# Kernel tuning notes

Hardware: AMD Instinct MI355X
Metric: run time of the kernel (lower is better)

Reference implementation:

```python
import jax, jax.numpy as jnp
import numpy as np

SEQ, B, OBS, H = 128, 256, 64, 1024

def setup_inputs() -> dict:
    key = jax.random.key(0)
    ks = jax.random.split(key, 16)
    s = 0.03  # keep weights small so tanh/sigmoid stay in a sane range
    n = lambda k, shape, sc=s: jax.random.normal(k, shape, jnp.float32) * sc
    return {
        "x": jax.random.normal(ks[0], (SEQ * B, OBS), jnp.float32),
        "done": jax.random.randint(ks[1], (SEQ * B,), 0, 2).astype(jnp.int32),
        "h0": n(ks[2], (2, B, H), 0.1),
        "c0": n(ks[3], (2, B, H), 0.1),
        "W_ih0": n(ks[4], (4 * H, OBS)),
        "W_hh0": n(ks[5], (4 * H, H)),
        "b_ih0": jnp.zeros((4 * H,), jnp.float32),
        "b_hh0": jnp.zeros((4 * H,), jnp.float32),
        "W_ih1": n(ks[6], (4 * H, H)),
        "W_hh1": n(ks[7], (4 * H, H)),
        "b_ih1": jnp.zeros((4 * H,), jnp.float32),
        "b_hh1": jnp.zeros((4 * H,), jnp.float32),
        "ln_g": jnp.ones((H,), jnp.float32),
        "ln_b": jnp.zeros((H,), jnp.float32),
        "W1": n(ks[8], (512, H)),
        "b1": jnp.zeros((512,), jnp.float32),
        "W2": n(ks[9], (128, 512)),
        "b2": jnp.zeros((128,), jnp.float32),
        "W3": n(ks[10], (64, 128)),
        "b3": jnp.zeros((64,), jnp.float32),
        "Wv": n(ks[11], (1, 64)),
        "bv": jnp.zeros((1,), jnp.float32),
    }

def _lstm_cell(xin, h, c, Wih, Whh, bih, bhh):
    # PyTorch gate order: input, forget, cell(g), output
    g = xin @ Wih.T + bih + h @ Whh.T + bhh
    i, f, gg, o = jnp.split(g, 4, axis=-1)
    c2 = jax.nn.sigmoid(f) * c + jax.nn.sigmoid(i) * jnp.tanh(gg)
    h2 = jax.nn.sigmoid(o) * jnp.tanh(c2)
    return h2, c2

def reference(x, done, h0, c0, W_ih0, W_hh0, b_ih0, b_hh0, W_ih1, W_hh1,
              b_ih1, b_hh1, ln_g, ln_b, W1, b1, W2, b2, W3, b3, Wv, bv):
    batch = h0.shape[1]
    obs = x.shape[-1]
    xs = x.reshape(-1, batch, obs)                      # (S, B, obs)
    ds = done.reshape(-1, batch).astype(x.dtype)        # (S, B)

    def step(carry, td):
        h, c = carry                                    # each (2, B, H)
        xt, dt = td
        m = (1.0 - dt)[:, None]                         # reset mask (B, 1)
        h0_, c0_ = _lstm_cell(xt, h[0] * m, c[0] * m, W_ih0, W_hh0, b_ih0, b_hh0)
        h1_, c1_ = _lstm_cell(h0_, h[1] * m, c[1] * m, W_ih1, W_hh1, b_ih1, b_hh1)
        return (jnp.stack([h0_, h1_]), jnp.stack([c0_, c1_])), h1_

    (hN, cN), hs = jax.lax.scan(step, (h0, c0), (xs, ds))
    hidden = hs.reshape(-1, hs.shape[-1])               # (S*B, H)

    # LayerNorm (eps = 1e-5, torch default)
    mu = hidden.mean(-1, keepdims=True)
    var = jnp.mean(jnp.square(hidden - mu), -1, keepdims=True)
    hn = (hidden - mu) * jax.lax.rsqrt(var + 1e-5) * ln_g + ln_b

    a = jax.nn.elu(hn @ W1.T + b1)
    a = jax.nn.elu(a @ W2.T + b2)
    a = jax.nn.elu(a @ W3.T + b3)
    value = a @ Wv.T + bv                               # (S*B, 1)
    return value, hN, cN
```

## Files before the change

### kernel.cpp

```cpp
#include <hip/hip_runtime.h>
#include <cstdint>
#include <cstddef>

typedef unsigned short u16;
typedef __attribute__((ext_vector_type(8))) short short8;
typedef __attribute__((ext_vector_type(4))) float f32x4;

#define SEQ 128
#define BATCH 256
#define HID 1024
#define LSZ 262144
#define RING 8

#define MFMA(a,b,c) __builtin_amdgcn_mfma_f32_16x16x32_bf16((a),(b),(c),0,0,0)

__device__ __forceinline__ u16 f2b(float f) {
  union { float f; unsigned u; } v; v.f = f;
  unsigned r = (v.u + 0x7FFFu + ((v.u >> 16) & 1u)) >> 16;
  return (u16)r;
}
__device__ __forceinline__ float b2f(u16 h) {
  union { unsigned u; float f; } v; v.u = ((unsigned)h) << 16; return v.f;
}
__device__ __forceinline__ float sigm(float x){ return 1.f/(1.f + __expf(-x)); }
__device__ __forceinline__ float tanh_f(float x){
  x = fminf(15.f, fmaxf(-15.f, x));
  float e = __expf(2.f*x); return (e-1.f)/(e+1.f);
}
__device__ __forceinline__ float eluf(float x){ return x > 0.f ? x : expm1f(x); }

__device__ __forceinline__ void gload(const u16* p, short8& d) {
  asm volatile("global_load_dwordx4 %0, %1, off" : "=&v"(d) : "v"(p) : "memory");
}
__device__ __forceinline__ void gload_nt(const u16* p, short8& d) {
  asm volatile("global_load_dwordx4 %0, %1, off nt" : "=&v"(d) : "v"(p) : "memory");
}
__device__ __forceinline__ void gload_cg(const u16* p, short8& d) {
  asm volatile("global_load_dwordx4 %0, %1, off sc0 sc1" : "=&v"(d) : "v"(p) : "memory");
}
__device__ __forceinline__ void store_cg(u16* p, short8 v) {
  asm volatile("global_store_dwordx4 %0, %1, off sc0 sc1" :: "v"(p), "v"(v) : "memory");
}
__device__ __forceinline__ void wait_vm0() {
  asm volatile("s_waitcnt vmcnt(0)" ::: "memory");
}
__device__ __forceinline__ void flag_set(int* p, int val) {
  asm volatile("global_store_dword %0, %1, off sc0 sc1" :: "v"(p), "v"(val) : "memory");
}
__device__ __forceinline__ void waitgroup(const int* f, int tgt) {
  if (threadIdx.x < 32) {
    const int* p = f + threadIdx.x * 32;
    while (true) {
      int v;
      asm volatile("global_load_dword %0, %1, off sc0 sc1\n\ts_waitcnt vmcnt(0)"
                   : "=v"(v) : "v"(p) : "memory");
      if (v >= tgt) break;
      __builtin_amdgcn_s_sleep(1);
    }
  }
  __syncthreads();
}

#define TIES_VB(vB) "+v"(vB[0][0]),"+v"(vB[0][1]),"+v"(vB[0][2]),"+v"(vB[0][3]), \
                    "+v"(vB[1][0]),"+v"(vB[1][1]),"+v"(vB[1][2]),"+v"(vB[1][3]), \
                    "+v"(vB[2][0]),"+v"(vB[2][1]),"+v"(vB[2][2]),"+v"(vB[2][3]), \
                    "+v"(vB[3][0]),"+v"(vB[3][1]),"+v"(vB[3][2]),"+v"(vB[3][3])
#define TIES_SV "+v"(sv[0]),"+v"(sv[1]),"+v"(sv[2]),"+v"(sv[3]),"+v"(sv[4]),"+v"(sv[5]),"+v"(sv[6]),"+v"(sv[7])

static const size_t OFF_W0F  = 0;
static const size_t OFF_W1F  = 8912896;
static const size_t OFF_XF   = 25690112;
static const size_t OFF_FLG  = 30932992;
static const size_t OFF_H1U  = 33030144;
static const size_t OFF_BS0  = 100663296;
static const size_t OFF_BS1  = 100679680;
static const size_t OFF_MU   = 100697088;
static const size_t OFF_RSTD = 100828160;
static const size_t OFF_W1LN = 100959232;
static const size_t OFF_S1   = 102007808;
static const size_t OFF_B1P  = 102009856;
static const size_t OFF_W2B  = 102011904;
static const size_t OFF_W3B  = 102142976;
static const size_t OFF_A1   = 102159360;
static const size_t OFF_H0R  = 102159360;
static const size_t OFF_A2   = 0;
static const size_t OFF_A3   = 8912896;

__global__ void prep_wf(const float* __restrict__ wih, const float* __restrict__ whh,
                        u16* __restrict__ out, int nkb, int kx) {
  int b = blockIdx.x; int cg = b >> 3, ct = b & 7;
  int g = ct >> 1;
  int n = nkb << 9;
  for (int e = threadIdx.x; e < n; e += 256) {
    int kb = e >> 9, r = e & 511;
    int q = r >> 7, col16 = (r >> 3) & 15, j = r & 7;
    int hl = (ct & 1) * 16 + col16;
    int gr = g * HID + cg * 32 + hl;
    int k = kb * 32 + q * 8 + j;
    float w = (k < kx) ? wih[(size_t)gr * kx + k] : whh[(size_t)gr * HID + (k - kx)];
    out[((size_t)(cg * nkb + kb) * 8 + ct) * 512 + r] = f2b(w);
  }
}

__global__ void prep_w1ln(const float* __restrict__ w1, const float* __restrict__ lng,
                          const float* __restrict__ lnb, const float* __restrict__ b1,
                          u16* __restrict__ w1ln, float* __restrict__ S1, float* __restrict__ b1p) {
  int j = blockIdx.x;
  float s = 0.f, bb = 0.f;
  for (int k = threadIdx.x; k < HID; k += 256) {
    float w = w1[(size_t)j * HID + k];
    u16 q = f2b(w * lng[k]);
    w1ln[(size_t)j * HID + k] = q;
    s += b2f(q);
    bb += w * lnb[k];
  }
  __shared__ float r1[256], r2[256];
  r1[threadIdx.x] = s; r2[threadIdx.x] = bb;
  __syncthreads();
  for (int o = 128; o > 0; o >>= 1) {
    if (threadIdx.x < (unsigned)o) { r1[threadIdx.x] += r1[threadIdx.x+o]; r2[threadIdx.x] += r2[threadIdx.x+o]; }
    __syncthreads();
  }
  if (threadIdx.x == 0) { S1[j] = r1[0]; b1p[j] = b1[j] + r2[0]; }
}

__global__ void prep_misc(const float* bih0, const float* bhh0, const float* bih1, const float* bhh1,
                          const float* x, const float* h0in,
                          const float* w2, const float* w3,
                          float* bs0, float* bs1, u16* xf, u16* h0r, u16* h1u,
                          u16* w2b, u16* w3b, int* flg) {
  size_t i = (size_t)blockIdx.x * blockDim.x + threadIdx.x;
  if (i < 4096) { bs0[i] = bih0[i] + bhh0[i]; return; }
  i -= 4096;
  if (i < 4096) { bs1[i] = bih1[i] + bhh1[i]; return; }
  i -= 4096;
  if (i < 2097152) {
    int o = (int)i;
    int r = o & 511, tile = o >> 9;
    int q = r >> 7, rl = (r >> 3) & 15, j = r & 7;
    int kb = tile & 1, v = tile >> 1;
    int grt = v & 15, t = v >> 4;
    int row = grt * 16 + rl, k = kb * 32 + q * 8 + j;
    xf[o] = f2b(x[((size_t)t * BATCH + row) * 64 + k]);
    return;
  }
  i -= 2097152;
  if (i < 262144) {
    int o = (int)i;
    int r = o & 511, tile = o >> 9;
    int q = r >> 7, rl = (r >> 3) & 15, j = r & 7;
    int grt = tile >> 5, kb = tile & 31;
    int row = grt * 16 + rl, h = kb * 32 + q * 8 + j;
    h0r[o] = f2b(h0in[(size_t)row * HID + h]);
    return;
  }
  i -= 262144;
  if (i < 262144) {
    int o = (int)i;
    int r = o & 511, tile = o >> 9;
    int q = r >> 7, rl = (r >> 3) & 15, j = r & 7;
    int grt = tile >> 5, kb = tile & 31;
    int row = grt * 16 + rl, h = kb * 32 + q * 8 + j;
    h1u[o] = f2b(h0in[LSZ + (size_t)row * HID + h]);
    return;
  }
  i -= 262144;
  if (i < 65536) { w2b[i] = f2b(w2[i]); return; }
  i -= 65536;
  if (i < 8192) { w3b[i] = f2b(w3[i]); return; }
  i -= 8192;
  if (i < 256) { flg[i * 32] = 0; return; }
}

__global__ __launch_bounds__(256, 1) void lstm_persist(
    const u16* __restrict__ w0f, const u16* __restrict__ w1f, const u16* __restrict__ xf,
    u16* __restrict__ h0r, u16* __restrict__ h1u,
    const float* __restrict__ c0all,
    const float* __restrict__ bs0, const float* __restrict__ bs1,
    const int* __restrict__ done, int* __restrict__ flg,
    float* __restrict__ dout)
{
  const int bid = blockIdx.x;
  const int layer = bid >> 7;
  const int rg = (bid >> 5) & 3;
  const int cg = bid & 31;
  const int tid = threadIdx.x;
  const int lane = tid & 63, wv = tid >> 6;
  const int wgr = wv & 1, wgc = wv >> 1;
  const int quad = lane >> 4, c16 = lane & 15;
  const int NKB = layer ? 64 : 34;
  const int NC  = layer ? 8 : 5;
  const int NH  = layer ? 16 : 9;
  const u16* Wf = layer ? w1f : w0f;
  const float* bs = layer ? bs1 : bs0;
  const float* cb = c0all + (size_t)layer * LSZ;
  int* fl0 = flg;
  int* fl1 = flg + 128 * 32;
  int* myf = (layer ? fl1 : fl0) + (rg * 32 + cg) * 32;
  int* g0 = fl0 + rg * 32 * 32;
  int* g1 = fl1 + rg * 32 * 32;

  __shared__ __align__(16) u16 smem[32768];
  float* gl = (float*)smem;

  const int sgrt = rg * 4 + wv;
  const int woff = (lane >> 4) * 128 + (lane & 15) * 8;
  const int srow = rg * 64 + wv * 16 + (lane & 15);
  const short8 z8 = {0,0,0,0,0,0,0,0};

  float creg[8];
  {
    const float* cp0 = cb + (size_t)(rg * 64 + (tid >> 2)) * HID + cg * 32 + (tid & 3) * 8;
    #pragma unroll
    for (int j = 0; j < 8; ++j) creg[j] = cp0[j];
  }

  for (int t = 0; t < SEQ; ++t) {
    if (layer == 0) {
      if (t >= RING) waitgroup(g1, t - (RING - 1));
      if (t >= 1)    waitgroup(g0, t);
    } else {
      waitgroup(g0, t + 1);
    }

    int sdone = done[t * BATCH + srow];
    asm volatile("" : "+v"(sdone));

    f32x4 acc0[4], acc1[4];
    #pragma unroll
    for (int i = 0; i < 4; ++i) { acc0[i] = (f32x4){0,0,0,0}; acc1[i] = (f32x4){0,0,0,0}; }
    short8 sv[8];
    short8 vBa[4][4], vBb[4][4];

    auto issueA = [&](int c) {
      int kb0 = c * 8;
      #pragma unroll
      for (int kbl = 0; kbl < 8; ++kbl) {
        int kb = kb0 + kbl;
        if (kb > NKB - 1) kb = NKB - 1;
        if (layer == 0) {
          if (kb < 2) {
            gload_nt(xf + ((size_t)((t * 16 + sgrt) * 2 + kb)) * 512 + woff, sv[kbl]);
          } else {
            gload_cg(h0r + (size_t)(t & (RING-1)) * 262144 + (size_t)(sgrt * 32 + (kb - 2)) * 512 + woff, sv[kbl]);
          }
        } else {
          if (kb < 32) {
            gload_cg(h0r + (size_t)((t + 1) & (RING-1)) * 262144 + (size_t)(sgrt * 32 + kb) * 512 + woff, sv[kbl]);
          } else {
            gload(h1u + (size_t)t * 262144 + (size_t)(sgrt * 32 + (kb - 32)) * 512 + woff, sv[kbl]);
          }
        }
      }
    };
    auto commitA = [&](int c) {
      int kb0 = c * 8;
      int bo = (c & 1) << 14;
      u16* d = &smem[bo + wv * 512 + woff];
      #pragma unroll
      for (int kbl = 0; kbl < 8; ++kbl) {
        int kb = kb0 + kbl;
        int maskable = layer ? (kb >= 32) : (kb >= 2);
        short8 v = sv[kbl];
        if (maskable && sdone) v = z8;
        *(short8*)(d + kbl * 2048) = v;
      }
    };
    auto issueB = [&](int h, short8 (&vB)[4][4]) {
      int kk = h * 4;
      #pragma unroll
      for (int kbl = 0; kbl < 4; ++kbl) {
        int kbx = kk + kbl;
        if (kbx > NKB - 1) kbx = NKB - 1;
        #pragma unroll
        for (int ct = 0; ct < 4; ++ct)
          gload(Wf + ((size_t)(cg * NKB + kbx) * 8 + wgc * 4 + ct) * 512 + lane * 8, vB[kbl][ct]);
      }
    };
    auto comp4 = [&](int h, short8 (&vB)[4][4]) {
      int kbc4 = NKB - h * 4; if (kbc4 > 4) kbc4 = 4;
      int bo = ((h >> 1) & 1) << 14;
      int tb = (h & 1) * 4;
      #pragma unroll
      for (int kbl = 0; kbl < 4; ++kbl) if (kbl < kbc4) {
        short8 af0 = *(const short8*)&smem[bo + ((tb + kbl) * 4 + wgr * 2 + 0) * 512 + lane * 8];
        short8 af1 = *(const short8*)&smem[bo + ((tb + kbl) * 4 + wgr * 2 + 1) * 512 + lane * 8];
        #pragma unroll
        for (int ct = 0; ct < 4; ++ct) {
          acc0[ct] = MFMA(af0, vB[kbl][ct], acc0[ct]);
          acc1[ct] = MFMA(af1, vB[kbl][ct], acc1[ct]);
        }
      }
    };

    issueB(0, vBa);
    issueA(0);
    issueB(1, vBb);
    asm volatile("s_waitcnt vmcnt(16)" : TIES_SV, TIES_VB(vBa) :: "memory");
    __builtin_amdgcn_sched_barrier(0);
    commitA(0);
    __syncthreads();

    for (int c = 0; c < NC - 1; ++c) {
      if (layer && c == 3 && t >= 1) waitgroup(g1, t);
      issueA(c + 1);
      comp4(2 * c, vBa);
      issueB(2 * c + 2, vBa);
      asm volatile("s_waitcnt vmcnt(24)" : TIES_VB(vBb) :: "memory");
      __builtin_amdgcn_sched_barrier(0);
      comp4(2 * c + 1, vBb);
      issueB(2 * c + 3, vBb);
      asm volatile("s_waitcnt vmcnt(32)" : TIES_SV :: "memory");
      __builtin_amdgcn_sched_barrier(0);
      commitA(c + 1);
      asm volatile("s_waitcnt vmcnt(16)" : TIES_VB(vBa) :: "memory");
      __builtin_amdgcn_sched_barrier(0);
      __syncthreads();
    }
    {
      int c = NC - 1;
      comp4(2 * c, vBa);
      asm volatile("s_waitcnt vmcnt(0)" : TIES_VB(vBb) :: "memory");
      __builtin_amdgcn_sched_barrier(0);
      if (2 * c + 1 < NH) comp4(2 * c + 1, vBb);
      __syncthreads();
    }

    #pragma unroll
    for (int ct = 0; ct < 4; ++ct)
      #pragma unroll
      for (int rgi = 0; rgi < 4; ++rgi) {
        int row0 = wgr * 32 + quad * 4 + rgi;
        int col = wgc * 64 + ct * 16 + c16;
        gl[row0 * 128 + col] = acc0[ct][rgi];
        gl[(row0 + 16) * 128 + col] = acc1[ct][rgi];
      }
    __syncthreads();

    {
      int row = tid >> 2;
      int q = tid & 3;
      int h8 = q * 8;
      int rowg = rg * 64 + row;
      int H0 = cg * 32 + h8;
      const float* glp = gl + row * 128;
      float m = done[t * BATCH + rowg] ? 0.f : 1.f;
      short8 hv;
      float h2a[8];
      #pragma unroll
      for (int j = 0; j < 8; ++j) {
        float ivv = glp[h8 + j]      + bs[H0 + j];
        float fvv = glp[32 + h8 + j] + bs[HID + H0 + j];
        float gvv = glp[64 + h8 + j] + bs[2*HID + H0 + j];
        float ovv = glp[96 + h8 + j] + bs[3*HID + H0 + j];
        float c2 = sigm(fvv) * (creg[j] * m) + sigm(ivv) * tanh_f(gvv);
        float h2 = sigm(ovv) * tanh_f(c2);
        creg[j] = c2;
        h2a[j] = h2;
        ((u16*)&hv)[j] = f2b(h2);
      }
      size_t off = (size_t)((rg * 4 + (row >> 4)) * 32 + cg) * 512 + (size_t)(q * 16 + (row & 15)) * 8;
      if (layer == 0) store_cg(h0r + (size_t)((t + 1) & (RING-1)) * 262144 + off, hv);
      else            store_cg(h1u + (size_t)(t + 1) * 262144 + off, hv);
      if (t == SEQ - 1) {
        float* dh = dout + 32768 + (size_t)layer * LSZ + (size_t)rowg * HID + H0;
        float* dc = dout + 32768 + 2 * LSZ + (size_t)layer * LSZ + (size_t)rowg * HID + H0;
        #pragma unroll
        for (int j = 0; j < 8; ++j) { dh[j] = h2a[j]; dc[j] = creg[j]; }
      }
    }
    wait_vm0();
    __syncthreads();
    if (tid == 0) flag_set(myf, t + 1);
  }
}

__global__ void ln_stats(const u16* __restrict__ h1u, float* __restrict__ mu, float* __restrict__ rstd) {
  int R = blockIdx.x * 4 + (threadIdx.x >> 6);
  int l = threadIdx.x & 63;
  int t = R >> 8, brow = R & 255, grt = brow >> 4, rl = brow & 15;
  const u16* base = h1u + (size_t)(t + 1) * 262144 + (size_t)(grt * 32 + (l >> 1)) * 512;
  int q2 = (l & 1) * 2;
  short8 v0 = *(const short8*)(base + (q2 * 16 + rl) * 8);
  short8 v1 = *(const short8*)(base + ((q2 + 1) * 16 + rl) * 8);
  float s = 0.f, q = 0.f;
  #pragma unroll
  for (int e = 0; e < 8; ++e) {
    float a = b2f((u16)v0[e]); s += a; q += a*a;
    float b = b2f((u16)v1[e]); s += b; q += b*b;
  }
  for (int o = 32; o > 0; o >>= 1) { s += __shfl_xor(s, o); q += __shfl_xor(q, o); }
  if (l == 0) {
    float mm = s * (1.f/1024.f);
    float var = q * (1.f/1024.f) - mm*mm;
    mu[R] = mm; rstd[R] = rsqrtf(var + 1e-5f);
  }
}

__global__ __launch_bounds__(512, 4) void mlp_gemm(
    const u16* __restrict__ A, int lda, int amode,
    const u16* __restrict__ B, int K, int N,
    u16* __restrict__ out, int ldo, int mode, int swiz,
    const float* __restrict__ mu, const float* __restrict__ rstd,
    const float* __restrict__ S1v, const float* __restrict__ bias)
{
  int nt, mtb;
  if (swiz) { int p = blockIdx.x * gridDim.y + blockIdx.y; nt = p & 3; mtb = p >> 2; }
  else { nt = blockIdx.x; mtb = blockIdx.y; }
  const int tid = threadIdx.x, lane = tid & 63, wv = tid >> 6;
  const int quad = lane >> 4, c16 = lane & 15;
  __shared__ __align__(16) u16 Am[16384], Bm[16384];
  f32x4 acc[8];
  #pragma unroll
  for (int i = 0; i < 8; ++i) acc[i] = (f32x4){0.f,0.f,0.f,0.f};

  int arow[4], akl[4], bcol[4];
  #pragma unroll
  for (int i = 0; i < 4; ++i) {
    int s = tid + i * 512, sub = s >> 6, lp = s & 63;
    int ks = sub >> 3, u = sub & 7;
    arow[i] = mtb * 128 + u * 16 + (lp & 15);
    akl[i]  = ks * 32 + (lp >> 4) * 8;
    bcol[i] = nt * 128 + u * 16 + (lp & 15);
  }
  short8 vA[4], vB[4];
  const short8 z8 = {0,0,0,0,0,0,0,0};
  const int NCH = K >> 7;
  auto load_stage = [&](int ci) {
    int kc = ci << 7;
    #pragma unroll
    for (int i = 0; i < 4; ++i) {
      if (amode) {
        int R = arow[i], k = kc + akl[i];
        const u16* p = A + (size_t)((R >> 8) + 1) * 262144
                         + (size_t)(((R >> 4) & 15) * 32 + (k >> 5)) * 512
                         + (size_t)((((k >> 3) & 3) * 16 + (R & 15)) * 8);
        vA[i] = *(const short8*)p;
      } else {
        vA[i] = *(const short8*)(A + (size_t)arow[i] * lda + kc + akl[i]);
      }
      vB[i] = (bcol[i] < N) ? *(const short8*)(B + (size_t)bcol[i] * K + kc + akl[i]) : z8;
    }
  };
  load_stage(0);
  for (int ci = 0; ci < NCH; ++ci) {
    #pragma unroll
    for (int i = 0; i < 4; ++i) {
      *(short8*)&Am[(size_t)(tid + i*512) * 8] = vA[i];
      *(short8*)&Bm[(size_t)(tid + i*512) * 8] = vB[i];
    }
    __syncthreads();
    if (ci + 1 < NCH) load_stage(ci + 1);
    #pragma unroll
    for (int ks = 0; ks < 4; ++ks) {
      short8 bf = *(const short8*)&Bm[((ks*8 + wv)*64 + lane) * 8];
      #pragma unroll
      for (int rt = 0; rt < 8; ++rt) {
        short8 af = *(const short8*)&Am[((ks*8 + rt)*64 + lane) * 8];
        acc[rt] = MFMA(af, bf, acc[rt]);
      }
    }
    __syncthreads();
  }
  int col = nt * 128 + wv * 16 + c16;
  if (col < N) {
    #pragma unroll
    for (int rt = 0; rt < 8; ++rt) {
      #pragma unroll
      for (int rgi = 0; rgi < 4; ++rgi) {
        int row = mtb * 128 + rt * 16 + quad * 4 + rgi;
        float v = acc[rt][rgi];
        if (mode == 0) v = v * rstd[row] - mu[row] * rstd[row] * S1v[col] + bias[col];
        else           v = v + bias[col];
        v = eluf(v);
        out[(size_t)row * ldo + col] = f2b(v);
      }
    }
  }
}

__global__ void value_head(const u16* __restrict__ a3, const float* __restrict__ wv,
                           const float* __restrict__ bv, float* __restrict__ dout) {
  int row = blockIdx.x * 256 + threadIdx.x;
  const short8* p = (const short8*)(a3 + (size_t)row * 64);
  float s = bv[0];
  #pragma unroll
  for (int j = 0; j < 8; ++j) {
    short8 v = p[j];
    #pragma unroll
    for (int e = 0; e < 8; ++e) s += b2f((u16)v[e]) * wv[j*8+e];
  }
  dout[row] = s;
}

extern "C" void kernel_launch(void* const* d_in, const int* in_sizes, int n_in,
                              void* d_out, int out_size, void* d_ws, size_t ws_size,
                              hipStream_t stream) {
  (void)in_sizes; (void)n_in; (void)out_size; (void)ws_size;
  const float* x    = (const float*)d_in[0];
  const int*   done = (const int*)d_in[1];
  const float* h0in = (const float*)d_in[2];
  const float* c0in = (const float*)d_in[3];
  const float* wih0 = (const float*)d_in[4];
  const float* whh0 = (const float*)d_in[5];
  const float* bih0 = (const float*)d_in[6];
  const float* bhh0 = (const float*)d_in[7];
  const float* wih1 = (const float*)d_in[8];
  const float* whh1 = (const float*)d_in[9];
  const float* bih1 = (const float*)d_in[10];
  const float* bhh1 = (const float*)d_in[11];
  const float* lng  = (const float*)d_in[12];
  const float* lnb  = (const float*)d_in[13];
  const float* w1   = (const float*)d_in[14];
  const float* b1   = (const float*)d_in[15];
  const float* w2   = (const float*)d_in[16];
  const float* b2   = (const float*)d_in[17];
  const float* w3   = (const float*)d_in[18];
  const float* b3   = (const float*)d_in[19];
  const float* wvp  = (const float*)d_in[20];
  const float* bvp  = (const float*)d_in[21];
  float* dout = (float*)d_out;
  char* ws = (char*)d_ws;

  u16*   w0f  = (u16*)(ws + OFF_W0F);
  u16*   w1f  = (u16*)(ws + OFF_W1F);
  u16*   xf   = (u16*)(ws + OFF_XF);
  u16*   h0r  = (u16*)(ws + OFF_H0R);
  u16*   h1u  = (u16*)(ws + OFF_H1U);
  float* bs0  = (float*)(ws + OFF_BS0);
  float* bs1  = (float*)(ws + OFF_BS1);
  int*   flg  = (int*)(ws + OFF_FLG);
  float* mu   = (float*)(ws + OFF_MU);
  float* rstd = (float*)(ws + OFF_RSTD);
  u16*   w1ln = (u16*)(ws + OFF_W1LN);
  float* s1   = (float*)(ws + OFF_S1);
  float* b1p  = (float*)(ws + OFF_B1P);
  u16*   w2b  = (u16*)(ws + OFF_W2B);
  u16*   w3b  = (u16*)(ws + OFF_W3B);
  u16*   a1   = (u16*)(ws + OFF_A1);
  u16*   a2   = (u16*)(ws + OFF_A2);
  u16*   a3   = (u16*)(ws + OFF_A3);

  prep_wf<<<256, 256, 0, stream>>>(wih0, whh0, w0f, 34, 64);
  prep_wf<<<256, 256, 0, stream>>>(wih1, whh1, w1f, 64, 1024);
  prep_w1ln<<<512, 256, 0, stream>>>(w1, lng, lnb, b1, w1ln, s1, b1p);
  prep_misc<<<12609, 256, 0, stream>>>(bih0, bhh0, bih1, bhh1, x, h0in, w2, w3,
                                       bs0, bs1, xf, h0r, h1u, w2b, w3b, flg);

  lstm_persist<<<256, 256, 0, stream>>>(w0f, w1f, xf, h0r, h1u, c0in,
                                        bs0, bs1, done, flg, dout);

  ln_stats<<<8192, 256, 0, stream>>>(h1u, mu, rstd);
  mlp_gemm<<<dim3(8, 128), 512, 0, stream>>>(h1u, 0, 1, w1ln, 1024, 512, a1, 512, 0, 1, mu, rstd, s1, b1p);
  mlp_gemm<<<dim3(1, 256), 512, 0, stream>>>(a1, 512, 0, w2b, 512, 128, a2, 128, 1, 0, mu, rstd, s1, b2);
  mlp_gemm<<<dim3(1, 256), 512, 0, stream>>>(a2, 128, 0, w3b, 128, 64, a3, 64, 1, 0, mu, rstd, s1, b3);
  value_head<<<128, 256, 0, stream>>>(a3, wvp, bvp, dout);
}
```

Baseline: 2.950 ms.

## Double LDS stage size to 16 k-blocks and halve per-timestep barriers

Restructures the per-timestep K loop of the persistent LSTM kernel so each LDS stage holds 16 k-blocks instead of 8. Shared memory doubles to 128 KB, which halves the number of __syncthreads per timestep, and the A-operand loads are split into two halves interleaved with the weight loads and MFMA groups. The aim is to cut barrier overhead and improve overlap of global loads with compute. In exchange, LDS occupancy rises and the vmcnt wait accounting becomes more intricate: issueB past the last k-block is clamped, and the final stage issues redundant loads.

```diff
diff --git a/kernel.cpp b/kernel.cpp
--- a/kernel.cpp
+++ b/kernel.cpp
@@ -65,7 +65,6 @@
                     "+v"(vB[1][0]),"+v"(vB[1][1]),"+v"(vB[1][2]),"+v"(vB[1][3]), \
                     "+v"(vB[2][0]),"+v"(vB[2][1]),"+v"(vB[2][2]),"+v"(vB[2][3]), \
                     "+v"(vB[3][0]),"+v"(vB[3][1]),"+v"(vB[3][2]),"+v"(vB[3][3])
-#define TIES_SV "+v"(sv[0]),"+v"(sv[1]),"+v"(sv[2]),"+v"(sv[3]),"+v"(sv[4]),"+v"(sv[5]),"+v"(sv[6]),"+v"(sv[7])
 
 static const size_t OFF_W0F  = 0;
 static const size_t OFF_W1F  = 8912896;
@@ -189,8 +188,7 @@
   const int wgr = wv & 1, wgc = wv >> 1;
   const int quad = lane >> 4, c16 = lane & 15;
   const int NKB = layer ? 64 : 34;
-  const int NC  = layer ? 8 : 5;
-  const int NH  = layer ? 16 : 9;
+  const int NC2 = layer ? 4 : 3;
   const u16* Wf = layer ? w1f : w0f;
   const float* bs = layer ? bs1 : bs0;
   const float* cb = c0all + (size_t)layer * LSZ;
@@ -200,13 +198,13 @@
   int* g0 = fl0 + rg * 32 * 32;
   int* g1 = fl1 + rg * 32 * 32;
 
-  __shared__ __align__(16) u16 smem[32768];
+  __shared__ __align__(16) u16 smem[65536];
   float* gl = (float*)smem;
 
   const int sgrt = rg * 4 + wv;
   const int woff = (lane >> 4) * 128 + (lane & 15) * 8;
-  const int srow = rg * 64 + wv * 16 + (lane & 15);
   const short8 z8 = {0,0,0,0,0,0,0,0};
+  (void)z8;
 
   float creg[8];
   {
@@ -223,7 +221,7 @@
       waitgroup(g0, t + 1);
     }
 
-    int sdone = done[t * BATCH + srow];
+    int sdone = done[t * BATCH + (rg * 64 + wv * 16 + (lane & 15))];
     asm volatile("" : "+v"(sdone));
 
     f32x4 acc0[4], acc1[4];
@@ -232,8 +230,8 @@
     short8 sv[8];
     short8 vBa[4][4], vBb[4][4];
 
-    auto issueA = [&](int c) {
-      int kb0 = c * 8;
+    auto issueA = [&](int c, int p) {
+      int kb0 = c * 16 + p * 8;
       #pragma unroll
       for (int kbl = 0; kbl < 8; ++kbl) {
         int kb = kb0 + kbl;
@@ -253,16 +251,16 @@
         }
       }
     };
-    auto commitA = [&](int c) {
-      int kb0 = c * 8;
-      int bo = (c & 1) << 14;
-      u16* d = &smem[bo + wv * 512 + woff];
+    auto commitA = [&](int c, int p) {
+      int kb0 = c * 16 + p * 8;
+      int bo = (c & 1) << 15;
+      u16* d = &smem[bo + (p * 32 + wv) * 512 + woff];
       #pragma unroll
       for (int kbl = 0; kbl < 8; ++kbl) {
         int kb = kb0 + kbl;
         int maskable = layer ? (kb >= 32) : (kb >= 2);
         short8 v = sv[kbl];
-        if (maskable && sdone) v = z8;
+        if (maskable && sdone) v = (short8){0,0,0,0,0,0,0,0};
         *(short8*)(d + kbl * 2048) = v;
       }
     };
@@ -279,8 +277,8 @@
     };
     auto comp4 = [&](int h, short8 (&vB)[4][4]) {
       int kbc4 = NKB - h * 4; if (kbc4 > 4) kbc4 = 4;
-      int bo = ((h >> 1) & 1) << 14;
-      int tb = (h & 1) * 4;
+      int bo = ((h >> 2) & 1) << 15;
+      int tb = (h & 3) * 4;
       #pragma unroll
       for (int kbl = 0; kbl < 4; ++kbl) if (kbl < kbc4) {
         short8 af0 = *(const short8*)&smem[bo + ((tb + kbl) * 4 + wgr * 2 + 0) * 512 + lane * 8];
@@ -293,36 +291,41 @@
       }
     };
 
+    issueA(0, 0);
     issueB(0, vBa);
-    issueA(0);
+    asm volatile("s_waitcnt vmcnt(16)" ::: "memory");
+    __builtin_amdgcn_sched_barrier(0);
+    commitA(0, 0);
+    issueA(0, 1);
     issueB(1, vBb);
-    asm volatile("s_waitcnt vmcnt(16)" : TIES_SV, TIES_VB(vBa) :: "memory");
+    asm volatile("s_waitcnt vmcnt(16)" : TIES_VB(vBa) :: "memory");
     __builtin_amdgcn_sched_barrier(0);
-    commitA(0);
+    commitA(0, 1);
     __syncthreads();
 
-    for (int c = 0; c < NC - 1; ++c) {
-      if (layer && c == 3 && t >= 1) waitgroup(g1, t);
-      issueA(c + 1);
-      comp4(2 * c, vBa);
-      issueB(2 * c + 2, vBa);
+    for (int c = 0; c < NC2; ++c) {
+      if (layer && c == 1 && t >= 1) waitgroup(g1, t);
+      int pre = (c + 1 < NC2);
+      comp4(4 * c, vBa);
+      issueB(4 * c + 2, vBa);
+      issueA(c + 1, 0);
       asm volatile("s_waitcnt vmcnt(24)" : TIES_VB(vBb) :: "memory");
       __builtin_amdgcn_sched_barrier(0);
-      comp4(2 * c + 1, vBb);
-      issueB(2 * c + 3, vBb);
-      asm volatile("s_waitcnt vmcnt(32)" : TIES_SV :: "memory");
-      __builtin_amdgcn_sched_barrier(0);
-      commitA(c + 1);
+      comp4(4 * c + 1, vBb);
+      issueB(4 * c + 3, vBb);
       asm volatile("s_waitcnt vmcnt(16)" : TIES_VB(vBa) :: "memory");
       __builtin_amdgcn_sched_barrier(0);
-      __syncthreads();
-    }
-    {
-      int c = NC - 1;
-      comp4(2 * c, vBa);
-      asm volatile("s_waitcnt vmcnt(0)" : TIES_VB(vBb) :: "memory");
+      if (pre) commitA(c + 1, 0);
+      issueA(c + 1, 1);
+      comp4(4 * c + 2, vBa);
+      issueB(4 * c + 4, vBa);
+      asm volatile("s_waitcnt vmcnt(16)" : TIES_VB(vBb) :: "memory");
       __builtin_amdgcn_sched_barrier(0);
-      if (2 * c + 1 < NH) comp4(2 * c + 1, vBb);
+      if (pre) commitA(c + 1, 1);
+      comp4(4 * c + 3, vBb);
+      issueB(4 * c + 5, vBb);
+      asm volatile("s_waitcnt vmcnt(16)" : TIES_VB(vBa) :: "memory");
+      __builtin_amdgcn_sched_barrier(0);
       __syncthreads();
     }
 
```

After: 3.091 ms. +4.8%, slower.

## Stage LSTM weight tiles into LDS via global_load_lds and rebalance wave tiling

Applied to the files above, without the earlier changes.

Recurrent weight fragments are now loaded straight from global memory into a double-buffered LDS region with global_load_lds, instead of into registers held across iterations. The wave layout also changes: each wave now owns 2 column tiles across all 4 row tiles, reading A from LDS per row tile. The goal is to cut register pressure and simplify the prefetch pipeline. The cost is double the shared memory, extra LDS reads per MFMA, and a pipeline where B staging depends on vmcnt and lgkmcnt waits. Those waits, the loop now running NC iterations, and cross-wave LDS visibility all risk races or stalls.

```diff
diff --git a/kernel.cpp b/kernel.cpp
--- a/kernel.cpp
+++ b/kernel.cpp
@@ -29,14 +29,19 @@
 }
 __device__ __forceinline__ float eluf(float x){ return x > 0.f ? x : expm1f(x); }
 
+__device__ __forceinline__ void gload_nt(const u16* p, short8& d) {
+  asm volatile("global_load_dwordx4 %0, %1, off nt" : "=&v"(d) : "v"(p) : "memory");
+}
+__device__ __forceinline__ void gload_cg(const u16* p, short8& d) {
+  asm volatile("global_load_dwordx4 %0, %1, off sc0 sc1" : "=&v"(d) : "v"(p) : "memory");
+}
 __device__ __forceinline__ void gload(const u16* p, short8& d) {
   asm volatile("global_load_dwordx4 %0, %1, off" : "=&v"(d) : "v"(p) : "memory");
 }
-__device__ __forceinline__ void gload_nt(const u16* p, short8& d) {
-  asm volatile("global_load_dwordx4 %0, %1, off nt" : "=&v"(d) : "v"(p) : "memory");
-}
-__device__ __forceinline__ void gload_cg(const u16* p, short8& d) {
-  asm volatile("global_load_dwordx4 %0, %1, off sc0 sc1" : "=&v"(d) : "v"(p) : "memory");
+__device__ __forceinline__ void gll16(const u16* gsrc, u16* ldst) {
+  __builtin_amdgcn_global_load_lds(
+      (const __attribute__((address_space(1))) unsigned int*)(const void*)gsrc,
+      (__attribute__((address_space(3))) unsigned int*)(void*)ldst, 16, 0, 0);
 }
 __device__ __forceinline__ void store_cg(u16* p, short8 v) {
   asm volatile("global_store_dwordx4 %0, %1, off sc0 sc1" :: "v"(p), "v"(v) : "memory");
@@ -61,10 +66,6 @@
   __syncthreads();
 }
 
-#define TIES_VB(vB) "+v"(vB[0][0]),"+v"(vB[0][1]),"+v"(vB[0][2]),"+v"(vB[0][3]), \
-                    "+v"(vB[1][0]),"+v"(vB[1][1]),"+v"(vB[1][2]),"+v"(vB[1][3]), \
-                    "+v"(vB[2][0]),"+v"(vB[2][1]),"+v"(vB[2][2]),"+v"(vB[2][3]), \
-                    "+v"(vB[3][0]),"+v"(vB[3][1]),"+v"(vB[3][2]),"+v"(vB[3][3])
 #define TIES_SV "+v"(sv[0]),"+v"(sv[1]),"+v"(sv[2]),"+v"(sv[3]),"+v"(sv[4]),"+v"(sv[5]),"+v"(sv[6]),"+v"(sv[7])
 
 static const size_t OFF_W0F  = 0;
@@ -186,11 +187,9 @@
   const int cg = bid & 31;
   const int tid = threadIdx.x;
   const int lane = tid & 63, wv = tid >> 6;
-  const int wgr = wv & 1, wgc = wv >> 1;
   const int quad = lane >> 4, c16 = lane & 15;
   const int NKB = layer ? 64 : 34;
   const int NC  = layer ? 8 : 5;
-  const int NH  = layer ? 16 : 9;
   const u16* Wf = layer ? w1f : w0f;
   const float* bs = layer ? bs1 : bs0;
   const float* cb = c0all + (size_t)layer * LSZ;
@@ -200,13 +199,14 @@
   int* g0 = fl0 + rg * 32 * 32;
   int* g1 = fl1 + rg * 32 * 32;
 
-  __shared__ __align__(16) u16 smem[32768];
+  __shared__ __align__(16) u16 smem[65536];
   float* gl = (float*)smem;
+  u16* smemB = smem + 32768;
 
   const int sgrt = rg * 4 + wv;
   const int woff = (lane >> 4) * 128 + (lane & 15) * 8;
-  const int srow = rg * 64 + wv * 16 + (lane & 15);
   const short8 z8 = {0,0,0,0,0,0,0,0};
+  (void)z8;
 
   float creg[8];
   {
@@ -223,14 +223,13 @@
       waitgroup(g0, t + 1);
     }
 
-    int sdone = done[t * BATCH + srow];
+    int sdone = done[t * BATCH + (rg * 64 + wv * 16 + (lane & 15))];
     asm volatile("" : "+v"(sdone));
 
-    f32x4 acc0[4], acc1[4];
-    #pragma unroll
-    for (int i = 0; i < 4; ++i) { acc0[i] = (f32x4){0,0,0,0}; acc1[i] = (f32x4){0,0,0,0}; }
+    f32x4 acc[4][2];
+    #pragma unroll
+    for (int i = 0; i < 4; ++i) { acc[i][0] = (f32x4){0,0,0,0}; acc[i][1] = (f32x4){0,0,0,0}; }
     short8 sv[8];
-    short8 vBa[4][4], vBb[4][4];
 
     auto issueA = [&](int c) {
       int kb0 = c * 8;
@@ -262,79 +261,74 @@
         int kb = kb0 + kbl;
         int maskable = layer ? (kb >= 32) : (kb >= 2);
         short8 v = sv[kbl];
-        if (maskable && sdone) v = z8;
+        if (maskable && sdone) v = (short8){0,0,0,0,0,0,0,0};
         *(short8*)(d + kbl * 2048) = v;
       }
     };
-    auto issueB = [&](int h, short8 (&vB)[4][4]) {
+    auto stageB = [&](int h) {
+      int sb = ((h & 1) << 14) + (wv << 12);
       int kk = h * 4;
       #pragma unroll
       for (int kbl = 0; kbl < 4; ++kbl) {
         int kbx = kk + kbl;
         if (kbx > NKB - 1) kbx = NKB - 1;
         #pragma unroll
-        for (int ct = 0; ct < 4; ++ct)
-          gload(Wf + ((size_t)(cg * NKB + kbx) * 8 + wgc * 4 + ct) * 512 + lane * 8, vB[kbl][ct]);
+        for (int ctl = 0; ctl < 2; ++ctl)
+          gll16(Wf + ((size_t)(cg * NKB + kbx) * 8 + wv * 2 + ctl) * 512 + lane * 8,
+                &smemB[sb + (kbl * 2 + ctl) * 512]);
       }
     };
-    auto comp4 = [&](int h, short8 (&vB)[4][4]) {
+    auto comp4 = [&](int h) {
       int kbc4 = NKB - h * 4; if (kbc4 > 4) kbc4 = 4;
       int bo = ((h >> 1) & 1) << 14;
       int tb = (h & 1) * 4;
+      int sb = ((h & 1) << 14) + (wv << 12);
       #pragma unroll
       for (int kbl = 0; kbl < 4; ++kbl) if (kbl < kbc4) {
-        short8 af0 = *(const short8*)&smem[bo + ((tb + kbl) * 4 + wgr * 2 + 0) * 512 + lane * 8];
-        short8 af1 = *(const short8*)&smem[bo + ((tb + kbl) * 4 + wgr * 2 + 1) * 512 + lane * 8];
+        short8 vb0 = *(const short8*)&smemB[sb + (kbl * 2 + 0) * 512 + lane * 8];
+        short8 vb1 = *(const short8*)&smemB[sb + (kbl * 2 + 1) * 512 + lane * 8];
         #pragma unroll
-        for (int ct = 0; ct < 4; ++ct) {
-          acc0[ct] = MFMA(af0, vB[kbl][ct], acc0[ct]);
-          acc1[ct] = MFMA(af1, vB[kbl][ct], acc1[ct]);
+        for (int r = 0; r < 4; ++r) {
+          short8 af = *(const short8*)&smem[bo + ((tb + kbl) * 4 + r) * 512 + lane * 8];
+          acc[r][0] = MFMA(af, vb0, acc[r][0]);
+          acc[r][1] = MFMA(af, vb1, acc[r][1]);
         }
       }
     };
 
-    issueB(0, vBa);
+    stageB(0);
     issueA(0);
-    issueB(1, vBb);
-    asm volatile("s_waitcnt vmcnt(16)" : TIES_SV, TIES_VB(vBa) :: "memory");
+    asm volatile("s_waitcnt vmcnt(0)" : TIES_SV :: "memory");
     __builtin_amdgcn_sched_barrier(0);
     commitA(0);
     __syncthreads();
 
-    for (int c = 0; c < NC - 1; ++c) {
+    for (int c = 0; c < NC; ++c) {
       if (layer && c == 3 && t >= 1) waitgroup(g1, t);
       issueA(c + 1);
-      comp4(2 * c, vBa);
-      issueB(2 * c + 2, vBa);
-      asm volatile("s_waitcnt vmcnt(24)" : TIES_VB(vBb) :: "memory");
+      stageB(2 * c + 1);
+      asm volatile("s_waitcnt vmcnt(16)" ::: "memory");
       __builtin_amdgcn_sched_barrier(0);
-      comp4(2 * c + 1, vBb);
-      issueB(2 * c + 3, vBb);
-      asm volatile("s_waitcnt vmcnt(32)" : TIES_SV :: "memory");
+      comp4(2 * c);
+      asm volatile("s_waitcnt lgkmcnt(0)" ::: "memory");
+      stageB(2 * c + 2);
+      asm volatile("s_waitcnt vmcnt(8)" : TIES_SV :: "memory");
       __builtin_amdgcn_sched_barrier(0);
-      commitA(c + 1);
-      asm volatile("s_waitcnt vmcnt(16)" : TIES_VB(vBa) :: "memory");
-      __builtin_amdgcn_sched_barrier(0);
+      if (c + 1 < NC) commitA(c + 1);
+      comp4(2 * c + 1);
       __syncthreads();
     }
-    {
-      int c = NC - 1;
-      comp4(2 * c, vBa);
-      asm volatile("s_waitcnt vmcnt(0)" : TIES_VB(vBb) :: "memory");
-      __builtin_amdgcn_sched_barrier(0);
-      if (2 * c + 1 < NH) comp4(2 * c + 1, vBb);
-      __syncthreads();
-    }
-
-    #pragma unroll
-    for (int ct = 0; ct < 4; ++ct)
-      #pragma unroll
-      for (int rgi = 0; rgi < 4; ++rgi) {
-        int row0 = wgr * 32 + quad * 4 + rgi;
-        int col = wgc * 64 + ct * 16 + c16;
-        gl[row0 * 128 + col] = acc0[ct][rgi];
-        gl[(row0 + 16) * 128 + col] = acc1[ct][rgi];
-      }
+
+    #pragma unroll
+    for (int r = 0; r < 4; ++r)
+      #pragma unroll
+      for (int ctl = 0; ctl < 2; ++ctl)
+        #pragma unroll
+        for (int rgi = 0; rgi < 4; ++rgi) {
+          int row0 = r * 16 + quad * 4 + rgi;
+          int col = wv * 32 + ctl * 16 + c16;
+          gl[row0 * 128 + col] = acc[r][ctl][rgi];
+        }
     __syncthreads();
 
     {
```

New measurement: 3.084 ms. 1.05x slower.

## Split layer-1 LSTM into input-projection and recurrent roles across extra blocks

Applied to the files above, without the earlier changes.

The persistent LSTM kernel grows from 256 to 384 blocks, with three roles. Layer 0 is unchanged. A new role computes the layer-1 input projection (h0 times W_ih1) ahead of time and writes the fp32 partial gates into a 4-slot ring buffer. The layer-1 recurrent role now only multiplies h1 by W_hh1, then adds the precomputed partials before the gate nonlinearities. This halves the K dimension on the serial layer-1 critical path, at the cost of more blocks, extra global traffic for the partials, and more flag synchronisation. It relies on two blocks per CU staying co-resident under the new launch bounds.

```diff
diff --git a/kernel.cpp b/kernel.cpp
--- a/kernel.cpp
+++ b/kernel.cpp
@@ -11,6 +11,7 @@
 #define HID 1024
 #define LSZ 262144
 #define RING 8
+#define RING_PG 4
 
 #define MFMA(a,b,c) __builtin_amdgcn_mfma_f32_16x16x32_bf16((a),(b),(c),0,0,0)
 
@@ -29,16 +30,22 @@
 }
 __device__ __forceinline__ float eluf(float x){ return x > 0.f ? x : expm1f(x); }
 
+__device__ __forceinline__ void gload_nt(const u16* p, short8& d) {
+  asm volatile("global_load_dwordx4 %0, %1, off nt" : "=&v"(d) : "v"(p) : "memory");
+}
+__device__ __forceinline__ void gload_cg(const u16* p, short8& d) {
+  asm volatile("global_load_dwordx4 %0, %1, off sc0 sc1" : "=&v"(d) : "v"(p) : "memory");
+}
+__device__ __forceinline__ void gload_cgf(const float* p, f32x4& d) {
+  asm volatile("global_load_dwordx4 %0, %1, off sc0 sc1" : "=&v"(d) : "v"(p) : "memory");
+}
 __device__ __forceinline__ void gload(const u16* p, short8& d) {
   asm volatile("global_load_dwordx4 %0, %1, off" : "=&v"(d) : "v"(p) : "memory");
 }
-__device__ __forceinline__ void gload_nt(const u16* p, short8& d) {
-  asm volatile("global_load_dwordx4 %0, %1, off nt" : "=&v"(d) : "v"(p) : "memory");
-}
-__device__ __forceinline__ void gload_cg(const u16* p, short8& d) {
-  asm volatile("global_load_dwordx4 %0, %1, off sc0 sc1" : "=&v"(d) : "v"(p) : "memory");
-}
 __device__ __forceinline__ void store_cg(u16* p, short8 v) {
+  asm volatile("global_store_dwordx4 %0, %1, off sc0 sc1" :: "v"(p), "v"(v) : "memory");
+}
+__device__ __forceinline__ void store_cgf(float* p, f32x4 v) {
   asm volatile("global_store_dwordx4 %0, %1, off sc0 sc1" :: "v"(p), "v"(v) : "memory");
 }
 __device__ __forceinline__ void wait_vm0() {
@@ -66,6 +73,7 @@
                     "+v"(vB[2][0]),"+v"(vB[2][1]),"+v"(vB[2][2]),"+v"(vB[2][3]), \
                     "+v"(vB[3][0]),"+v"(vB[3][1]),"+v"(vB[3][2]),"+v"(vB[3][3])
 #define TIES_SV "+v"(sv[0]),"+v"(sv[1]),"+v"(sv[2]),"+v"(sv[3]),"+v"(sv[4]),"+v"(sv[5]),"+v"(sv[6]),"+v"(sv[7])
+#define TIES_PV "+v"(pv[0]),"+v"(pv[1]),"+v"(pv[2]),"+v"(pv[3]),"+v"(pv[4]),"+v"(pv[5]),"+v"(pv[6]),"+v"(pv[7])
 
 static const size_t OFF_W0F  = 0;
 static const size_t OFF_W1F  = 8912896;
@@ -83,6 +91,7 @@
 static const size_t OFF_W3B  = 102142976;
 static const size_t OFF_A1   = 102159360;
 static const size_t OFF_H0R  = 102159360;
+static const size_t OFF_PG   = 106353664;
 static const size_t OFF_A2   = 0;
 static const size_t OFF_A3   = 8912896;
 
@@ -169,62 +178,70 @@
   i -= 65536;
   if (i < 8192) { w3b[i] = f2b(w3[i]); return; }
   i -= 8192;
-  if (i < 256) { flg[i * 32] = 0; return; }
-}
-
-__global__ __launch_bounds__(256, 1) void lstm_persist(
+  if (i < 384) { flg[i * 32] = 0; return; }
+}
+
+__global__ __launch_bounds__(256, 2) void lstm_persist(
     const u16* __restrict__ w0f, const u16* __restrict__ w1f, const u16* __restrict__ xf,
-    u16* __restrict__ h0r, u16* __restrict__ h1u,
+    u16* __restrict__ h0r, u16* __restrict__ h1u, float* __restrict__ pg,
     const float* __restrict__ c0all,
     const float* __restrict__ bs0, const float* __restrict__ bs1,
     const int* __restrict__ done, int* __restrict__ flg,
     float* __restrict__ dout)
 {
   const int bid = blockIdx.x;
-  const int layer = bid >> 7;
+  const int role = bid >> 7;
   const int rg = (bid >> 5) & 3;
   const int cg = bid & 31;
   const int tid = threadIdx.x;
   const int lane = tid & 63, wv = tid >> 6;
   const int wgr = wv & 1, wgc = wv >> 1;
   const int quad = lane >> 4, c16 = lane & 15;
-  const int NKB = layer ? 64 : 34;
-  const int NC  = layer ? 8 : 5;
-  const int NH  = layer ? 16 : 9;
-  const u16* Wf = layer ? w1f : w0f;
-  const float* bs = layer ? bs1 : bs0;
-  const float* cb = c0all + (size_t)layer * LSZ;
-  int* fl0 = flg;
-  int* fl1 = flg + 128 * 32;
-  int* myf = (layer ? fl1 : fl0) + (rg * 32 + cg) * 32;
-  int* g0 = fl0 + rg * 32 * 32;
-  int* g1 = fl1 + rg * 32 * 32;
+  const int NKB = (role == 0) ? 34 : 32;
+  const int NC  = (role == 0) ? 5 : 4;
+  const int NH  = (role == 0) ? 9 : 8;
+  const u16* Wf = (role == 0) ? w0f : w1f;
+  const int wtb = (role == 0) ? cg * 34 : cg * 64 + ((role == 1) ? 32 : 0);
+  const float* bs = (role == 0) ? bs0 : bs1;
+  int* fl0  = flg;
+  int* fl1b = flg + 4096;
+  int* fl1a = flg + 8192;
+  int* myf = ((role == 0) ? fl0 : (role == 1) ? fl1b : fl1a) + (rg * 32 + cg) * 32;
+  int* g0  = fl0  + rg * 32 * 32;
+  int* g1b = fl1b + rg * 32 * 32;
+  int* g1a = fl1a + rg * 32 * 32;
 
   __shared__ __align__(16) u16 smem[32768];
   float* gl = (float*)smem;
 
   const int sgrt = rg * 4 + wv;
   const int woff = (lane >> 4) * 128 + (lane & 15) * 8;
-  const int srow = rg * 64 + wv * 16 + (lane & 15);
-  const short8 z8 = {0,0,0,0,0,0,0,0};
+  float* pgblk = pg + (size_t)(rg * 32 + cg) * 8192 + (size_t)tid * 32;
 
   float creg[8];
-  {
-    const float* cp0 = cb + (size_t)(rg * 64 + (tid >> 2)) * HID + cg * 32 + (tid & 3) * 8;
+  if (role != 2) {
+    const float* cp0 = c0all + (size_t)((role == 1) ? 1 : 0) * LSZ
+                     + (size_t)(rg * 64 + (tid >> 2)) * HID + cg * 32 + (tid & 3) * 8;
     #pragma unroll
     for (int j = 0; j < 8; ++j) creg[j] = cp0[j];
   }
 
   for (int t = 0; t < SEQ; ++t) {
-    if (layer == 0) {
-      if (t >= RING) waitgroup(g1, t - (RING - 1));
+    if (role == 0) {
+      if (t >= RING) waitgroup(g1a, t - (RING - 1));
       if (t >= 1)    waitgroup(g0, t);
+    } else if (role == 2) {
+      waitgroup(g0, t + 1);
+      if (t >= RING_PG) waitgroup(g1b, t - (RING_PG - 1));
     } else {
-      waitgroup(g0, t + 1);
-    }
-
-    int sdone = done[t * BATCH + srow];
-    asm volatile("" : "+v"(sdone));
+      if (t >= 1) waitgroup(g1b, t);
+    }
+
+    int sdone = 0;
+    if (role != 2) {
+      sdone = done[t * BATCH + (rg * 64 + wv * 16 + (lane & 15))];
+      asm volatile("" : "+v"(sdone));
+    }
 
     f32x4 acc0[4], acc1[4];
     #pragma unroll
@@ -238,18 +255,16 @@
       for (int kbl = 0; kbl < 8; ++kbl) {
         int kb = kb0 + kbl;
         if (kb > NKB - 1) kb = NKB - 1;
-        if (layer == 0) {
+        if (role == 0) {
           if (kb < 2) {
             gload_nt(xf + ((size_t)((t * 16 + sgrt) * 2 + kb)) * 512 + woff, sv[kbl]);
           } else {
             gload_cg(h0r + (size_t)(t & (RING-1)) * 262144 + (size_t)(sgrt * 32 + (kb - 2)) * 512 + woff, sv[kbl]);
           }
+        } else if (role == 2) {
+          gload_cg(h0r + (size_t)((t + 1) & (RING-1)) * 262144 + (size_t)(sgrt * 32 + kb) * 512 + woff, sv[kbl]);
         } else {
-          if (kb < 32) {
-            gload_cg(h0r + (size_t)((t + 1) & (RING-1)) * 262144 + (size_t)(sgrt * 32 + kb) * 512 + woff, sv[kbl]);
-          } else {
-            gload(h1u + (size_t)t * 262144 + (size_t)(sgrt * 32 + (kb - 32)) * 512 + woff, sv[kbl]);
-          }
+          gload(h1u + (size_t)t * 262144 + (size_t)(sgrt * 32 + kb) * 512 + woff, sv[kbl]);
         }
       }
     };
@@ -260,9 +275,9 @@
       #pragma unroll
       for (int kbl = 0; kbl < 8; ++kbl) {
         int kb = kb0 + kbl;
-        int maskable = layer ? (kb >= 32) : (kb >= 2);
+        int maskable = (role == 0) ? (kb >= 2) : (role == 1);
         short8 v = sv[kbl];
-        if (maskable && sdone) v = z8;
+        if (maskable && sdone) v = (short8){0,0,0,0,0,0,0,0};
         *(short8*)(d + kbl * 2048) = v;
       }
     };
@@ -274,7 +289,7 @@
         if (kbx > NKB - 1) kbx = NKB - 1;
         #pragma unroll
         for (int ct = 0; ct < 4; ++ct)
-          gload(Wf + ((size_t)(cg * NKB + kbx) * 8 + wgc * 4 + ct) * 512 + lane * 8, vB[kbl][ct]);
+          gload(Wf + ((size_t)(wtb + kbx) * 8 + wgc * 4 + ct) * 512 + lane * 8, (short8&)vB[kbl][ct]);
       }
     };
     auto comp4 = [&](int h, short8 (&vB)[4][4]) {
@@ -302,7 +317,6 @@
     __syncthreads();
 
     for (int c = 0; c < NC - 1; ++c) {
-      if (layer && c == 3 && t >= 1) waitgroup(g1, t);
       issueA(c + 1);
       comp4(2 * c, vBa);
       issueB(2 * c + 2, vBa);
@@ -326,6 +340,32 @@
       __syncthreads();
     }
 
+    if (role == 2) {
+      float* pgt = pgblk + (size_t)(t & (RING_PG - 1)) * 1048576;
+      store_cgf(pgt + 0,  acc0[0]); store_cgf(pgt + 4,  acc0[1]);
+      store_cgf(pgt + 8,  acc0[2]); store_cgf(pgt + 12, acc0[3]);
+      store_cgf(pgt + 16, acc1[0]); store_cgf(pgt + 20, acc1[1]);
+      store_cgf(pgt + 24, acc1[2]); store_cgf(pgt + 28, acc1[3]);
+      wait_vm0();
+      __syncthreads();
+      if (tid == 0) flag_set(myf, t + 1);
+      continue;
+    }
+
+    if (role == 1) {
+      waitgroup(g1a, t + 1);
+      const float* pgt = pgblk + (size_t)(t & (RING_PG - 1)) * 1048576;
+      f32x4 pv[8];
+      gload_cgf(pgt + 0,  pv[0]); gload_cgf(pgt + 4,  pv[1]);
+      gload_cgf(pgt + 8,  pv[2]); gload_cgf(pgt + 12, pv[3]);
+      gload_cgf(pgt + 16, pv[4]); gload_cgf(pgt + 20, pv[5]);
+      gload_cgf(pgt + 24, pv[6]); gload_cgf(pgt + 28, pv[7]);
+      asm volatile("s_waitcnt vmcnt(0)" : TIES_PV :: "memory");
+      __builtin_amdgcn_sched_barrier(0);
+      #pragma unroll
+      for (int ct = 0; ct < 4; ++ct) { acc0[ct] += pv[ct]; acc1[ct] += pv[4 + ct]; }
+    }
+
     #pragma unroll
     for (int ct = 0; ct < 4; ++ct)
       #pragma unroll
@@ -360,11 +400,12 @@
         ((u16*)&hv)[j] = f2b(h2);
       }
       size_t off = (size_t)((rg * 4 + (row >> 4)) * 32 + cg) * 512 + (size_t)(q * 16 + (row & 15)) * 8;
-      if (layer == 0) store_cg(h0r + (size_t)((t + 1) & (RING-1)) * 262144 + off, hv);
-      else            store_cg(h1u + (size_t)(t + 1) * 262144 + off, hv);
+      if (role == 0) store_cg(h0r + (size_t)((t + 1) & (RING-1)) * 262144 + off, hv);
+      else           store_cg(h1u + (size_t)(t + 1) * 262144 + off, hv);
       if (t == SEQ - 1) {
-        float* dh = dout + 32768 + (size_t)layer * LSZ + (size_t)rowg * HID + H0;
-        float* dc = dout + 32768 + 2 * LSZ + (size_t)layer * LSZ + (size_t)rowg * HID + H0;
+        int lyr = (role == 1) ? 1 : 0;
+        float* dh = dout + 32768 + (size_t)lyr * LSZ + (size_t)rowg * HID + H0;
+        float* dc = dout + 32768 + 2 * LSZ + (size_t)lyr * LSZ + (size_t)rowg * HID + H0;
         #pragma unroll
         for (int j = 0; j < 8; ++j) { dh[j] = h2a[j]; dc[j] = creg[j]; }
       }
@@ -527,6 +568,7 @@
   u16*   xf   = (u16*)(ws + OFF_XF);
   u16*   h0r  = (u16*)(ws + OFF_H0R);
   u16*   h1u  = (u16*)(ws + OFF_H1U);
+  float* pg   = (float*)(ws + OFF_PG);
   float* bs0  = (float*)(ws + OFF_BS0);
   float* bs1  = (float*)(ws + OFF_BS1);
   int*   flg  = (int*)(ws + OFF_FLG);
@@ -547,7 +589,7 @@
   prep_misc<<<12609, 256, 0, stream>>>(bih0, bhh0, bih1, bhh1, x, h0in, w2, w3,
                                        bs0, bs1, xf, h0r, h1u, w2b, w3b, flg);
 
-  lstm_persist<<<256, 256, 0, stream>>>(w0f, w1f, xf, h0r, h1u, c0in,
+  lstm_persist<<<384, 256, 0, stream>>>(w0f, w1f, xf, h0r, h1u, pg, c0in,
                                         bs0, bs1, done, flg, dout);
 
   ln_stats<<<8192, 256, 0, stream>>>(h1u, mu, rstd);
```

Result: slower. 4.019 ms (+36.2%).
